# Kernel tuning notes

Hardware: AMD Instinct MI355X
Metric: run time of the kernel (lower is better)

Reference implementation:

```python
import jax, jax.numpy as jnp
import numpy as np

K = 4  # knn_graph(k=4, loop=False) hard-coded in H2GCN.forward


def _knn_2hop_adj(Fet, k):
    """Per-batch kNN graph -> symmetrize -> 2-hop binary adjacency [B,N,N].

    Matches create_adj + get_2hop_neighbors: edge direction and the row
    normalization in create_adj are irrelevant because get_2hop_neighbors
    symmetrizes (adj[row,col]=adj[col,row]=1) and thresholds (adj@adj > 0).
    """
    B, N, _ = Fet.shape
    sq = jnp.sum(Fet * Fet, axis=-1)  # [B,N]
    dist = sq[:, :, None] + sq[:, None, :] - 2.0 * jnp.einsum('bnf,bmf->bnm', Fet, Fet)
    eye = jnp.eye(N, dtype=bool)
    dist = jnp.where(eye[None], jnp.inf, dist)  # loop=False: exclude self
    _, idx = jax.lax.top_k(-dist, k)  # [B,N,k] nearest-neighbor indices
    b_idx = jnp.arange(B)[:, None, None]
    n_idx = jnp.arange(N)[None, :, None]
    A = jnp.zeros((B, N, N), Fet.dtype).at[b_idx, n_idx, idx].set(1.0)
    A = jnp.maximum(A, jnp.swapaxes(A, 1, 2))  # symmetrize 1-hop
    A2 = jnp.einsum('bnm,bmk->bnk', A, A)      # 2-hop counts
    A2 = jnp.where(eye[None], 0.0, A2)          # fill_diagonal_(0)
    return (A2 > 0).astype(Fet.dtype)


def _h2gcn_conv(x, A2, w1, b1, w2, b2):
    """H2GCNConv on dense binary adjacency.

    Dense matmul with binary A2 == gather(x[col]) -> fc2 -> index_add over rows;
    A2.sum(-1) == bincount(row). Degree clamped to >= 1.
    """
    ego = jnp.einsum('bnf,of->bno', x, w1) + b1   # fc1(x)
    msg = jnp.einsum('bnf,of->bno', x, w2) + b2   # fc2(x)
    agg = jnp.einsum('bnm,bmo->bno', A2, msg)     # scatter-add of neighbor msgs
    deg = jnp.maximum(jnp.sum(A2, axis=-1, keepdims=True), 1.0)
    return jax.nn.relu(jnp.concatenate([ego, agg / deg], axis=-1))


def setup_inputs() -> dict:
    key = jax.random.key(0)
    ks = jax.random.split(key, 8)
    B, N, F, NH, NC = 128, 197, 768, 512, 1000
    s = 0.02
    return {
        'Fet': jax.random.normal(ks[0], (B, N, F), jnp.float32),
        'w1_0': jax.random.normal(ks[1], (NH, F), jnp.float32) * s,
        'b1_0': jnp.zeros((NH,), jnp.float32),
        'w2_0': jax.random.normal(ks[2], (NH, F), jnp.float32) * s,
        'b2_0': jnp.zeros((NH,), jnp.float32),
        'w1_1': jax.random.normal(ks[3], (NH, 2 * NH), jnp.float32) * s,
        'b1_1': jnp.zeros((NH,), jnp.float32),
        'w2_1': jax.random.normal(ks[4], (NH, 2 * NH), jnp.float32) * s,
        'b2_1': jnp.zeros((NH,), jnp.float32),
        'fc1_w': jax.random.normal(ks[5], (NH, 4 * NH), jnp.float32) * s,
        'fc1_b': jnp.zeros((NH,), jnp.float32),
        'fc2_w': jax.random.normal(ks[6], (NC, NH), jnp.float32) * s,
        'fc2_b': jnp.zeros((NC,), jnp.float32),
    }


def reference(Fet, w1_0, b1_0, w2_0, b2_0, w1_1, b1_1, w2_1, b2_1,
              fc1_w, fc1_b, fc2_w, fc2_b):
    A2 = _knn_2hop_adj(Fet, K)
    h1 = _h2gcn_conv(Fet, A2, w1_0, b1_0, w2_0, b2_0)   # [B,N,2*nhid]
    h2 = _h2gcn_conv(h1, A2, w1_1, b1_1, w2_1, b2_1)    # [B,N,2*nhid]
    h = jnp.concatenate([h1, h2], axis=-1)              # [B,N,final_dim]
    graph_features = jnp.mean(h, axis=1)                # global_mean_pool
    p = jax.nn.relu(graph_features @ fc1_w.T + fc1_b)   # dropout is identity (eval)
    out = p @ fc2_w.T + fc2_b
    return (out, graph_features)
```

## Files before the change

### kernel.cpp

```cpp
#include <hip/hip_runtime.h>
#include <hip/hip_bf16.h>
#include <math.h>

typedef __attribute__((ext_vector_type(8))) short bf16x8;
typedef __attribute__((ext_vector_type(4))) float f32x4;

#define B_ 128
#define N_ 197
#define F_ 768
#define NH_ 512
#define D2_ 1024
#define D4_ 2048
#define NC_ 1000
#define ROWS_ (B_ * N_)
#define KA_ 224
#define NA_ 256
#define LDG_ 200
#define MT_LD_ (B_ * KA_)

#define OFF_G0     0ull
#define OFF_SQ     20172800ull
#define OFF_ABITS  20273664ull
#define OFF_DEG    21080576ull
#define OFF_FETHI  21181440ull
#define OFF_MSGT   60011520ull
#define OFF_H1     89371648ull
#define OFF_FETLO  OFF_MSGT
#define OFF_POOL   141014016ull
#define OFF_P      142062592ull
#define OFF_WC1    142324736ull
#define OFF_WC2    143897600ull
#define OFF_G1     145994752ull

__device__ __forceinline__ void gll16(const void* g, void* l) {
  __builtin_amdgcn_global_load_lds((const __attribute__((address_space(1))) void*)g,
                                   (__attribute__((address_space(3))) void*)l, 16, 0, 0);
}


__global__ __launch_bounds__(256) void cast_weights(const float* __restrict__ w10,
                                                    const float* __restrict__ w20,
                                                    const float* __restrict__ w11,
                                                    const float* __restrict__ w21,
                                                    __hip_bfloat16* __restrict__ wc1,
                                                    __hip_bfloat16* __restrict__ wc2) {
  const int S1 = NH_ * F_ / 4;
  const int S2 = NH_ * D2_ / 4;
  int i = blockIdx.x * 256 + threadIdx.x;
  const float* src;
  __hip_bfloat16* dst;
  int off;
  if (i < S1) { src = w10; dst = wc1; off = i; }
  else if (i < 2 * S1) { src = w20; dst = wc1 + (size_t)NH_ * F_; off = i - S1; }
  else if (i < 2 * S1 + S2) { src = w11; dst = wc2; off = i - 2 * S1; }
  else { src = w21; dst = wc2 + (size_t)NH_ * D2_; off = i - 2 * S1 - S2; }
  float4 v = ((const float4*)src)[off];
  union { __hip_bfloat16 h[4]; uint2 u; } pk;
  pk.h[0] = __float2bfloat16(v.x);
  pk.h[1] = __float2bfloat16(v.y);
  pk.h[2] = __float2bfloat16(v.z);
  pk.h[3] = __float2bfloat16(v.w);
  ((uint2*)dst)[off] = pk.u;
}

__global__ __launch_bounds__(256) void cast_hilo_sq(const float* __restrict__ X,
                                                    __hip_bfloat16* __restrict__ hi,
                                                    __hip_bfloat16* __restrict__ lo,
                                                    float* __restrict__ sq) {
  int row = blockIdx.x * 4 + (threadIdx.x >> 6);
  int lane = threadIdx.x & 63;
  const float4* xp = (const float4*)(X + (size_t)row * F_);
  uint2* hp = (uint2*)(hi + (size_t)row * F_);
  uint2* lp = (uint2*)(lo + (size_t)row * F_);
  float s = 0.f;
#pragma unroll
  for (int i = 0; i < 3; i++) {
    float4 v = xp[lane + i * 64];
    s += v.x * v.x + v.y * v.y + v.z * v.z + v.w * v.w;
    float f[4] = {v.x, v.y, v.z, v.w};
    union { __hip_bfloat16 h[4]; uint2 u; } ph, pl;
#pragma unroll
    for (int k = 0; k < 4; k++) {
      __hip_bfloat16 h = __float2bfloat16(f[k]);
      ph.h[k] = h;
      pl.h[k] = __float2bfloat16(f[k] - __bfloat162float(h));
    }
    hp[lane + i * 64] = ph.u;
    lp[lane + i * 64] = pl.u;
  }
#pragma unroll
  for (int o = 32; o > 0; o >>= 1) s += __shfl_down(s, o);
  if (lane == 0) sq[row] = s;
}

__global__ __launch_bounds__(256) void mfma_gram(const __hip_bfloat16* __restrict__ Xhi,
                                                 const __hip_bfloat16* __restrict__ Xlo,
                                                 float* __restrict__ g0,
                                                 float* __restrict__ g1) {
  __shared__ short AsH[4096];
  __shared__ short BsH[4096];
  __shared__ short AsL[4096];
  __shared__ short BsL[4096];
  const int t = threadIdx.x;
  const int wgid = blockIdx.x;
  const int L = (wgid & 7) * 96 + (wgid >> 3);
  const int b = L / 6;
  const int rbx = L - b * 6;
  const int bx = rbx % 3;
  const int khalf = rbx / 3;
  const int m0 = (bx == 0) ? 0 : 128;
  const int o0 = (bx == 2) ? 128 : 0;
  const bool mirror = (bx == 1);
  const int l = t & 63, w = t >> 6;
  const int wm = (w >> 1) * 64, wn = (w & 1) * 64;
  const int frow = l & 15, fch = l >> 4;
  const size_t rowbase = (size_t)b * N_;
  const char* AhiB = (const char*)(Xhi + (rowbase + m0) * F_);
  const char* AloB = (const char*)(Xlo + (rowbase + m0) * F_);
  const char* BhiB = (const char*)(Xhi + (rowbase + o0) * F_);
  const char* BloB = (const char*)(Xlo + (rowbase + o0) * F_);
  const int rb = F_ * 2;
  char* AsHB = (char*)AsH;
  char* BsHB = (char*)BsH;
  char* AsLB = (char*)AsL;
  char* BsLB = (char*)BsL;
  float* go = khalf ? g1 : g0;
  f32x4 zero = {0.f, 0.f, 0.f, 0.f};
  f32x4 acc[4][4];
#pragma unroll
  for (int i = 0; i < 4; i++)
#pragma unroll
    for (int j = 0; j < 4; j++) acc[i][j] = zero;
  const int kt0 = khalf * 12;
  for (int kt = kt0; kt < kt0 + 12; kt++) {
    const int kb = kt * 64;
#pragma unroll
    for (int u = 0; u < 2; u++) {
      int prow = u * 32 + (t >> 3);
      int e = (t & 7) ^ (prow & 7);
      int grow = (e >> 2) * 64 + prow;
      size_t goff = (size_t)grow * rb + kb + (e & 3) * 16;
      gll16(AhiB + goff, AsHB + u * 4096 + t * 16);
      gll16(BhiB + goff, BsHB + u * 4096 + t * 16);
      gll16(AloB + goff, AsLB + u * 4096 + t * 16);
      gll16(BloB + goff, BsLB + u * 4096 + t * 16);
    }
    __syncthreads();
    bf16x8 ah[4], al[4], bh[4], bl[4];
#pragma unroll
    for (int i = 0; i < 4; i++) {
      int ar = wm + i * 16 + frow;
      int apr = ar & 63;
      int aoff = apr * 128 + (((((ar >> 6) << 2) | fch) ^ (apr & 7)) * 16);
      ah[i] = *(const bf16x8*)(AsHB + aoff);
      al[i] = *(const bf16x8*)(AsLB + aoff);
      int br = wn + i * 16 + frow;
      int bpr = br & 63;
      int boff = bpr * 128 + (((((br >> 6) << 2) | fch) ^ (bpr & 7)) * 16);
      bh[i] = *(const bf16x8*)(BsHB + boff);
      bl[i] = *(const bf16x8*)(BsLB + boff);
    }
#pragma unroll
    for (int i = 0; i < 4; i++)
#pragma unroll
      for (int j = 0; j < 4; j++) {
        acc[i][j] = __builtin_amdgcn_mfma_f32_16x16x32_bf16(bh[j], ah[i], acc[i][j], 0, 0, 0);
        acc[i][j] = __builtin_amdgcn_mfma_f32_16x16x32_bf16(bl[j], ah[i], acc[i][j], 0, 0, 0);
        acc[i][j] = __builtin_amdgcn_mfma_f32_16x16x32_bf16(bh[j], al[i], acc[i][j], 0, 0, 0);
      }
    __syncthreads();
  }
#pragma unroll
  for (int i = 0; i < 4; i++) {
    int n = m0 + wm + i * 16 + frow;
    if (n >= N_) continue;
    float* gr = go + (rowbase + n) * LDG_;
#pragma unroll
    for (int j = 0; j < 4; j++) {
      int mb = o0 + wn + j * 16 + fch * 4;
      if (mb >= LDG_) continue;
      f32x4 pv = acc[i][j];
      *(f32x4*)&gr[mb] = pv;
      if (mirror) {
#pragma unroll
        for (int r = 0; r < 4; r++)
          go[(rowbase + mb + r) * LDG_ + n] = pv[r];
      }
    }
  }
}

__global__ __launch_bounds__(256) void topk_kernel(const float* __restrict__ g0,
                                                   const float* __restrict__ g1,
                                                   const float* __restrict__ sq,
                                                   unsigned long long* __restrict__ Abits) {
  int row = blockIdx.x * 4 + (threadIdx.x >> 6);
  int lane = threadIdx.x & 63;
  int b = row / N_, n = row - b * N_;
  const float* g0r = g0 + (size_t)row * LDG_;
  const float* g1r = g1 + (size_t)row * LDG_;
  const float* sqb = sq + (size_t)b * N_;
  float v[4];
  int vi[4];
#pragma unroll
  for (int i = 0; i < 4; i++) {
    int m = lane + i * 64;
    bool ok = (m < N_) && (m != n);
    v[i] = ok ? (sqb[m] - 2.f * (g0r[m] + g1r[m])) : INFINITY;
    vi[i] = ok ? m : 0x3fffffff;
  }
  unsigned long long nbr[4] = {0ull, 0ull, 0ull, 0ull};
#pragma unroll
  for (int t = 0; t < 4; t++) {
    float bv = v[0];
    int bi = vi[0];
#pragma unroll
    for (int i = 1; i < 4; i++)
      if (v[i] < bv || (v[i] == bv && vi[i] < bi)) { bv = v[i]; bi = vi[i]; }
#pragma unroll
    for (int o = 1; o < 64; o <<= 1) {
      float ov = __shfl_xor(bv, o);
      int oi = __shfl_xor(bi, o);
      if (ov < bv || (ov == bv && oi < bi)) { bv = ov; bi = oi; }
    }
#pragma unroll
    for (int i = 0; i < 4; i++)
      if (vi[i] == bi) { v[i] = INFINITY; vi[i] = 0x3fffffff; }
    if (lane == 0) {
      nbr[bi >> 6] |= 1ull << (bi & 63);
      atomicOr(&Abits[((size_t)b * N_ + bi) * 4 + (n >> 6)], 1ull << (n & 63));
    }
  }
  if (lane == 0) {
#pragma unroll
    for (int w = 0; w < 4; w++)
      if (nbr[w]) atomicOr(&Abits[(size_t)row * 4 + w], nbr[w]);
  }
}

__global__ __launch_bounds__(256) void a2_kernel(const unsigned long long* __restrict__ Abits,
                                                 __hip_bfloat16* __restrict__ A2bf,
                                                 float* __restrict__ deg) {
  int row = blockIdx.x * 4 + (threadIdx.x >> 6);
  int lane = threadIdx.x & 63;
  int b = row / N_, n = row - b * N_;
  const unsigned long long* arow = Abits + (size_t)row * 4;
  const unsigned long long* base = Abits + (size_t)b * N_ * 4;
  unsigned long long r0 = 0, r1 = 0, r2 = 0, r3 = 0;
#pragma unroll
  for (int w = 0; w < 4; w++) {
    if ((arow[w] >> lane) & 1ull) {
      const unsigned long long* mr = base + (size_t)(w * 64 + lane) * 4;
      r0 |= mr[0]; r1 |= mr[1]; r2 |= mr[2]; r3 |= mr[3];
    }
  }
#pragma unroll
  for (int o = 1; o < 64; o <<= 1) {
    r0 |= __shfl_xor(r0, o);
    r1 |= __shfl_xor(r1, o);
    r2 |= __shfl_xor(r2, o);
    r3 |= __shfl_xor(r3, o);
  }
  unsigned long long rr[4] = {r0, r1, r2, r3};
  rr[n >> 6] &= ~(1ull << (n & 63));
  const int pad = b & 3;
  __hip_bfloat16* out = A2bf + ((size_t)b * NA_ + n) * KA_;
  const __hip_bfloat16 one = __float2bfloat16(1.f);
  const __hip_bfloat16 zer = __float2bfloat16(0.f);
#pragma unroll
  for (int i = 0; i < 4; i++) {
    int m = lane + i * 64;
    if (m < KA_) {
      int k = m - pad;
      bool bit = (k >= 0 && k < N_ && ((rr[k >> 6] >> (k & 63)) & 1ull));
      out[m] = bit ? one : zer;
    }
  }
  if (lane == 0) {
    int dg = __popcll(rr[0]) + __popcll(rr[1]) + __popcll(rr[2]) + __popcll(rr[3]);
    deg[row] = (float)(dg > 0 ? dg : 1);
  }
}

template <int MODE>
__global__ __launch_bounds__(256) void mfma_fused(const __hip_bfloat16* __restrict__ X,
                                                  const __hip_bfloat16* __restrict__ Wcat,
                                                  const float* __restrict__ biasE,
                                                  const float* __restrict__ biasM,
                                                  __hip_bfloat16* __restrict__ h1,
                                                  __hip_bfloat16* __restrict__ msgT,
                                                  float* __restrict__ pool,
                                                  int K) {
  __shared__ short As[2][4096];
  __shared__ short Bs[2][4096];
  const int t = threadIdx.x;
  const int wgid = blockIdx.x;
  const int L = (wgid & 7) * 197 + (wgid >> 3);
  const int m0 = (L >> 3) * 128, o0 = (L & 7) * 128;
  const int l = t & 63, w = t >> 6;
  const int wm = (w >> 1) * 64, wn = (w & 1) * 64;
  const int frow = l & 15, fch = l >> 4;
  const char* Abase = (const char*)(X + (size_t)m0 * K);
  const char* Bbase = (const char*)(Wcat + (size_t)o0 * K);
  const int rb = K * 2;
  char* AsB = (char*)As;
  char* BsB = (char*)Bs;
  const bool ego = (o0 < 512);
  const bool swap = (MODE == 1) && ego;
  const int sp = t >> 3;
  const int se = (t & 7) ^ (sp & 7);
  const size_t goff0 = (size_t)((se >> 2) * 64 + sp) * rb + (se & 3) * 16;
  const size_t goff1 = (size_t)((se >> 2) * 64 + 32 + sp) * rb + (se & 3) * 16;
  auto stage = [&](int buf, int kt) {
    const int kb = kt * 64;
    const int d = buf * 8192 + t * 16;
    gll16(Abase + goff0 + kb, AsB + d);
    gll16(Abase + goff1 + kb, AsB + d + 4096);
    gll16(Bbase + goff0 + kb, BsB + d);
    gll16(Bbase + goff1 + kb, BsB + d + 4096);
  };
  f32x4 zero = {0.f, 0.f, 0.f, 0.f};
  f32x4 acc[4][4];
#pragma unroll
  for (int i = 0; i < 4; i++)
#pragma unroll
    for (int j = 0; j < 4; j++) acc[i][j] = zero;
  const int KT = K >> 5;
  stage(0, 0);
  __syncthreads();
  for (int kt = 0; kt < KT; kt++) {
    const int cur = kt & 1;
    if (kt + 1 < KT) stage(cur ^ 1, kt + 1);
    bf16x8 af[4], bfv[4];
#pragma unroll
    for (int i = 0; i < 4; i++) {
      int ar = wm + i * 16 + frow;
      int apr = ar & 63;
      af[i] = *(const bf16x8*)(AsB + cur * 8192 + apr * 128 +
                               (((((ar >> 6) << 2) | fch) ^ (apr & 7)) * 16));
      int br = wn + i * 16 + frow;
      int bpr = br & 63;
      bfv[i] = *(const bf16x8*)(BsB + cur * 8192 + bpr * 128 +
                                (((((br >> 6) << 2) | fch) ^ (bpr & 7)) * 16));
    }
    if (!swap) {
#pragma unroll
      for (int i = 0; i < 4; i++)
#pragma unroll
        for (int j = 0; j < 4; j++)
          acc[i][j] = __builtin_amdgcn_mfma_f32_16x16x32_bf16(af[i], bfv[j], acc[i][j], 0, 0, 0);
    } else {
#pragma unroll
      for (int i = 0; i < 4; i++)
#pragma unroll
        for (int j = 0; j < 4; j++)
          acc[i][j] = __builtin_amdgcn_mfma_f32_16x16x32_bf16(bfv[j], af[i], acc[i][j], 0, 0, 0);
    }
    __syncthreads();
  }
  if (ego) {
    if (MODE == 1) {
      const int rw = m0 + wm;
      const int b0 = rw / N_;
      const int rloc = (b0 + 1) * N_ - rw;
#pragma unroll
      for (int j = 0; j < 4; j++) {
        int c0 = o0 + wn + j * 16 + fch * 4;
        float4 b4 = *(const float4*)&biasE[c0];
        float bb4[4] = {b4.x, b4.y, b4.z, b4.w};
        float sA4[4] = {0.f, 0.f, 0.f, 0.f};
        float sB4[4] = {0.f, 0.f, 0.f, 0.f};
#pragma unroll
        for (int i = 0; i < 4; i++) {
          int xloc = i * 16 + frow;
          union { __hip_bfloat16 h[4]; uint2 u; } pk;
#pragma unroll
          for (int r = 0; r < 4; r++) {
            float v = fmaxf(acc[i][j][r] + bb4[r], 0.f);
            pk.h[r] = __float2bfloat16(v);
            if (xloc < rloc) sA4[r] += v; else sB4[r] += v;
          }
          *(uint2*)&h1[(size_t)(rw + xloc) * D2_ + c0] = pk.u;
        }
#pragma unroll
        for (int r = 0; r < 4; r++) {
          float sA = sA4[r], sB = sB4[r];
          sA += __shfl_down(sA, 8, 16); sA += __shfl_down(sA, 4, 16);
          sA += __shfl_down(sA, 2, 16); sA += __shfl_down(sA, 1, 16);
          sB += __shfl_down(sB, 8, 16); sB += __shfl_down(sB, 4, 16);
          sB += __shfl_down(sB, 2, 16); sB += __shfl_down(sB, 1, 16);
          if ((l & 15) == 0) {
            atomicAdd(&pool[(size_t)b0 * D4_ + c0 + r], sA);
            if (rloc < 64) atomicAdd(&pool[(size_t)(b0 + 1) * D4_ + c0 + r], sB);
          }
        }
      }
    } else {
#pragma unroll
      for (int j = 0; j < 4; j++) {
        int c = o0 + wn + j * 16 + frow;
        float bv = biasE[c];
        int rw = m0 + wm;
        int b0 = rw / N_;
        int rB = (b0 + 1) * N_;
        float sA = 0.f, sB = 0.f;
#pragma unroll
        for (int i = 0; i < 4; i++) {
          int r0 = m0 + wm + i * 16 + fch * 4;
#pragma unroll
          for (int r = 0; r < 4; r++) {
            float v = fmaxf(acc[i][j][r] + bv, 0.f);
            if (r0 + r < rB) sA += v; else sB += v;
          }
        }
        sA += __shfl_down(sA, 32);
        sA += __shfl_down(sA, 16);
        sB += __shfl_down(sB, 32);
        sB += __shfl_down(sB, 16);
        if (l < 16) {
          atomicAdd(&pool[(size_t)b0 * D4_ + D2_ + c], sA);
          if (rw + 64 > rB) atomicAdd(&pool[(size_t)(b0 + 1) * D4_ + D2_ + c], sB);
        }
      }
    }
  } else {
#pragma unroll
    for (int j = 0; j < 4; j++) {
      int cm = (o0 - 512) + wn + j * 16 + frow;
      float bm = biasM[cm];
      __hip_bfloat16* mrow = msgT + (size_t)cm * MT_LD_;
#pragma unroll
      for (int i = 0; i < 4; i++) {
        int x0 = m0 + wm + i * 16 + fch * 4;
        int b0 = x0 / N_;
        int r0 = x0 - b0 * N_;
        union { __hip_bfloat16 h[4]; uint2 u; } pk;
#pragma unroll
        for (int r = 0; r < 4; r++) pk.h[r] = __float2bfloat16(acc[i][j][r] + bm);
        if (r0 + 3 < N_) {
          *(uint2*)&mrow[b0 * KA_ + (b0 & 3) + r0] = pk.u;
        } else {
#pragma unroll
          for (int r = 0; r < 4; r++) {
            int x = x0 + r;
            int bb = x / N_;
            int rx = x - bb * N_;
            mrow[bb * KA_ + (bb & 3) + rx] = pk.h[r];
          }
        }
      }
    }
  }
}

template <int MODE>
__global__ __launch_bounds__(256) void mfma_agg(const __hip_bfloat16* __restrict__ A2bf,
                                                const __hip_bfloat16* __restrict__ msgT,
                                                const float* __restrict__ deg,
                                                __hip_bfloat16* __restrict__ h1,
                                                float* __restrict__ pool, int poolOff) {
  __shared__ short As[2][4096];
  __shared__ short Bs[2][4096];
  const int t = threadIdx.x;
  const int wgid = blockIdx.x;
  const int L = (wgid & 7) * 128 + (wgid >> 3);
  const int b = L >> 3;
  const int o0 = ((L >> 1) & 3) * 128;
  const int m0 = (L & 1) * 128;
  const int l = t & 63, w = t >> 6;
  const int wm = (w >> 1) * 64, wn = (w & 1) * 64;
  const int frow = l & 15, fch = l >> 4;
  const char* Abase = (const char*)(A2bf + ((size_t)b * NA_ + m0) * KA_);
  const char* Bbase = (const char*)(msgT + (size_t)o0 * MT_LD_ + (size_t)b * KA_);
  char* AsB = (char*)As;
  char* BsB = (char*)Bs;
  const int sp = t >> 3;
  const int se = (t & 7) ^ (sp & 7);
  const int sg0 = (se >> 2) * 64 + sp;
  const int sg1 = sg0 + 32;
  const int sx = (se & 3) * 16;
  auto stage = [&](int buf, int kt) {
    const int kb = kt * 64;
    const int d = buf * 8192 + t * 16;
    gll16(Abase + (size_t)sg0 * (KA_ * 2) + kb + sx, AsB + d);
    gll16(Abase + (size_t)sg1 * (KA_ * 2) + kb + sx, AsB + d + 4096);
    gll16(Bbase + (size_t)sg0 * (MT_LD_ * 2) + kb + sx, BsB + d);
    gll16(Bbase + (size_t)sg1 * (MT_LD_ * 2) + kb + sx, BsB + d + 4096);
  };
  f32x4 zero = {0.f, 0.f, 0.f, 0.f};
  f32x4 acc[4][4];
#pragma unroll
  for (int i = 0; i < 4; i++)
#pragma unroll
    for (int j = 0; j < 4; j++) acc[i][j] = zero;
  stage(0, 0);
  __syncthreads();
  for (int kt = 0; kt < 7; kt++) {
    const int cur = kt & 1;
    if (kt + 1 < 7) stage(cur ^ 1, kt + 1);
    bf16x8 af[4], bfv[4];
#pragma unroll
    for (int i = 0; i < 4; i++) {
      int ar = wm + i * 16 + frow;
      int apr = ar & 63;
      af[i] = *(const bf16x8*)(AsB + cur * 8192 + apr * 128 +
                               (((((ar >> 6) << 2) | fch) ^ (apr & 7)) * 16));
      int br = wn + i * 16 + frow;
      int bpr = br & 63;
      bfv[i] = *(const bf16x8*)(BsB + cur * 8192 + bpr * 128 +
                                (((((br >> 6) << 2) | fch) ^ (bpr & 7)) * 16));
    }
#pragma unroll
    for (int i = 0; i < 4; i++)
#pragma unroll
      for (int j = 0; j < 4; j++)
        acc[i][j] = __builtin_amdgcn_mfma_f32_16x16x32_bf16(bfv[j], af[i], acc[i][j], 0, 0, 0);
    __syncthreads();
  }
  float sv[4][4];
#pragma unroll
  for (int j = 0; j < 4; j++)
#pragma unroll
    for (int r = 0; r < 4; r++) sv[j][r] = 0.f;
#pragma unroll
  for (int i = 0; i < 4; i++) {
    int n = m0 + wm + i * 16 + frow;
    bool ok = (n < N_);
    float dinv = ok ? (1.f / deg[b * N_ + n]) : 0.f;
#pragma unroll
    for (int j = 0; j < 4; j++) {
      int c0 = o0 + wn + j * 16 + fch * 4;
      union { __hip_bfloat16 h[4]; uint2 u; } pk;
#pragma unroll
      for (int r = 0; r < 4; r++) {
        float v = ok ? fmaxf(acc[i][j][r] * dinv, 0.f) : 0.f;
        sv[j][r] += v;
        pk.h[r] = __float2bfloat16(v);
      }
      if (MODE == 0 && ok)
        *(uint2*)&h1[((size_t)b * N_ + n) * D2_ + NH_ + c0] = pk.u;
    }
  }
#pragma unroll
  for (int j = 0; j < 4; j++) {
#pragma unroll
    for (int r = 0; r < 4; r++) {
      float s = sv[j][r];
      s += __shfl_down(s, 8, 16);
      s += __shfl_down(s, 4, 16);
      s += __shfl_down(s, 2, 16);
      s += __shfl_down(s, 1, 16);
      if ((l & 15) == 0)
        atomicAdd(&pool[(size_t)b * D4_ + poolOff + o0 + wn + j * 16 + fch * 4 + r], s);
    }
  }
}

__global__ __launch_bounds__(256) void scale_pool(const float* __restrict__ pool,
                                                  float* __restrict__ gf) {
  int b = blockIdx.y;
  int c = blockIdx.x * 256 + threadIdx.x;
  gf[(size_t)b * D4_ + c] = pool[(size_t)b * D4_ + c] * (1.f / N_);
}

template <bool RELUX>
__global__ __launch_bounds__(256) void head_gemm(const float* __restrict__ Xg,
                                                 const float* __restrict__ W,
                                                 const float* __restrict__ bias,
                                                 float* __restrict__ Y,
                                                 int Rows, int Fin, int O, int kchunk) {
  __shared__ float Xs[16][68];
  __shared__ float Ws[16][68];
  int tx = threadIdx.x, ty = threadIdx.y;
  int tid = ty * 16 + tx;
  int lr = tid >> 2;
  int lk = (tid & 3) * 4;
  int rbase = blockIdx.y * 64;
  int o0 = blockIdx.x * 64;
  int k0base = blockIdx.z * kchunk;
  float acc[4][4] = {};
  for (int k0 = k0base; k0 < k0base + kchunk; k0 += 16) {
    float4 xv = make_float4(0.f, 0.f, 0.f, 0.f);
    if (rbase + lr < Rows) xv = *(const float4*)&Xg[(size_t)(rbase + lr) * Fin + k0 + lk];
    if (RELUX) {
      xv.x = fmaxf(xv.x, 0.f); xv.y = fmaxf(xv.y, 0.f);
      xv.z = fmaxf(xv.z, 0.f); xv.w = fmaxf(xv.w, 0.f);
    }
    Xs[lk][lr] = xv.x; Xs[lk + 1][lr] = xv.y; Xs[lk + 2][lr] = xv.z; Xs[lk + 3][lr] = xv.w;
    float4 wv = make_float4(0.f, 0.f, 0.f, 0.f);
    if (o0 + lr < O) wv = *(const float4*)&W[(size_t)(o0 + lr) * Fin + k0 + lk];
    Ws[lk][lr] = wv.x; Ws[lk + 1][lr] = wv.y; Ws[lk + 2][lr] = wv.z; Ws[lk + 3][lr] = wv.w;
    __syncthreads();
#pragma unroll
    for (int k = 0; k < 16; k++) {
      float4 a = *(const float4*)&Xs[k][ty * 4];
      float4 bb = *(const float4*)&Ws[k][tx * 4];
      float av[4] = {a.x, a.y, a.z, a.w};
      float bv[4] = {bb.x, bb.y, bb.z, bb.w};
#pragma unroll
      for (int i = 0; i < 4; i++)
#pragma unroll
        for (int j = 0; j < 4; j++) acc[i][j] = fmaf(av[i], bv[j], acc[i][j]);
    }
    __syncthreads();
  }
#pragma unroll
  for (int i = 0; i < 4; i++) {
    int rrow = rbase + ty * 4 + i;
    if (rrow >= Rows) continue;
#pragma unroll
    for (int j = 0; j < 4; j++) {
      int c = o0 + tx * 4 + j;
      if (c >= O) continue;
      float vv = acc[i][j] + ((blockIdx.z == 0) ? bias[c] : 0.f);
      atomicAdd(&Y[(size_t)rrow * O + c], vv);
    }
  }
}

extern "C" void kernel_launch(void* const* d_in, const int* in_sizes, int n_in,
                              void* d_out, int out_size, void* d_ws, size_t ws_size,
                              hipStream_t stream) {
  const float* Fet  = (const float*)d_in[0];
  const float* w1_0 = (const float*)d_in[1];
  const float* b1_0 = (const float*)d_in[2];
  const float* w2_0 = (const float*)d_in[3];
  const float* b2_0 = (const float*)d_in[4];
  const float* w1_1 = (const float*)d_in[5];
  const float* b1_1 = (const float*)d_in[6];
  const float* w2_1 = (const float*)d_in[7];
  const float* b2_1 = (const float*)d_in[8];
  const float* fc1_w = (const float*)d_in[9];
  const float* fc1_b = (const float*)d_in[10];
  const float* fc2_w = (const float*)d_in[11];
  const float* fc2_b = (const float*)d_in[12];

  char* ws = (char*)d_ws;
  float* g0 = (float*)(ws + OFF_G0);
  float* g1 = (float*)(ws + OFF_G1);
  __hip_bfloat16* A2bf = (__hip_bfloat16*)(ws + OFF_G0);
  float* sq = (float*)(ws + OFF_SQ);
  unsigned long long* Abits = (unsigned long long*)(ws + OFF_ABITS);
  float* deg = (float*)(ws + OFF_DEG);
  __hip_bfloat16* Fet_hi = (__hip_bfloat16*)(ws + OFF_FETHI);
  __hip_bfloat16* Fet_lo = (__hip_bfloat16*)(ws + OFF_FETLO);
  __hip_bfloat16* msgT = (__hip_bfloat16*)(ws + OFF_MSGT);
  __hip_bfloat16* h1 = (__hip_bfloat16*)(ws + OFF_H1);
  float* pool = (float*)(ws + OFF_POOL);
  float* p = (float*)(ws + OFF_P);
  __hip_bfloat16* wc1 = (__hip_bfloat16*)(ws + OFF_WC1);
  __hip_bfloat16* wc2 = (__hip_bfloat16*)(ws + OFF_WC2);

  float* out = (float*)d_out;
  float* gf = out + (size_t)B_ * NC_;

  hipMemsetAsync(Abits, 0, (size_t)ROWS_ * 4 * sizeof(unsigned long long), stream);
  hipMemsetAsync(pool, 0, (size_t)B_ * D4_ * sizeof(float), stream);
  hipMemsetAsync(p, 0, (size_t)B_ * NH_ * sizeof(float), stream);
  hipMemsetAsync(out, 0, (size_t)B_ * NC_ * sizeof(float), stream);

  cast_hilo_sq<<<ROWS_ / 4, 256, 0, stream>>>(Fet, Fet_hi, Fet_lo, sq);
  cast_weights<<<1792, 256, 0, stream>>>(w1_0, w2_0, w1_1, w2_1, wc1, wc2);

  mfma_gram<<<768, 256, 0, stream>>>(Fet_hi, Fet_lo, g0, g1);
  topk_kernel<<<ROWS_ / 4, 256, 0, stream>>>(g0, g1, sq, Abits);
  a2_kernel<<<ROWS_ / 4, 256, 0, stream>>>(Abits, A2bf, deg);

  mfma_fused<1><<<1576, 256, 0, stream>>>(Fet_hi, wc1, b1_0, b2_0, h1, msgT, pool, F_);
  mfma_agg<0><<<1024, 256, 0, stream>>>(A2bf, msgT, deg, h1, pool, NH_);

  mfma_fused<2><<<1576, 256, 0, stream>>>(h1, wc2, b1_1, b2_1, nullptr, msgT, pool, D2_);
  mfma_agg<1><<<1024, 256, 0, stream>>>(A2bf, msgT, deg, nullptr, pool, D2_ + NH_);

  scale_pool<<<dim3(8, B_), 256, 0, stream>>>(pool, gf);

  head_gemm<false><<<dim3(8, 2, 16), dim3(16, 16), 0, stream>>>(
      gf, fc1_w, fc1_b, p, B_, D4_, NH_, 128);
  head_gemm<true><<<dim3(16, 2, 8), dim3(16, 16), 0, stream>>>(
      p, fc2_w, fc2_b, out, B_, NH_, NC_, 64);
}
```

Baseline: 440.7 us.

## Enlarge fused GEMM tiles to 256x256 with 8 waves and interleaved prefetch

```diff
diff --git a/kernel.cpp b/kernel.cpp
--- a/kernel.cpp
+++ b/kernel.cpp
@@ -13,6 +13,8 @@
 #define D4_ 2048
 #define NC_ 1000
 #define ROWS_ (B_ * N_)
+#define MPAD_ 25344
+#define GRIDM_ 99
 #define KA_ 224
 #define NA_ 256
 #define LDG_ 200
@@ -23,20 +25,19 @@
 #define OFF_ABITS  20273664ull
 #define OFF_DEG    21080576ull
 #define OFF_FETHI  21181440ull
-#define OFF_MSGT   60011520ull
-#define OFF_H1     89371648ull
+#define OFF_MSGT   60109824ull
+#define OFF_H1     89469952ull
 #define OFF_FETLO  OFF_MSGT
-#define OFF_POOL   141014016ull
-#define OFF_P      142062592ull
-#define OFF_WC1    142324736ull
-#define OFF_WC2    143897600ull
-#define OFF_G1     145994752ull
+#define OFF_POOL   141374464ull
+#define OFF_P      142423040ull
+#define OFF_WC1    142685184ull
+#define OFF_WC2    144258048ull
+#define OFF_G1     146355200ull
 
 __device__ __forceinline__ void gll16(const void* g, void* l) {
   __builtin_amdgcn_global_load_lds((const __attribute__((address_space(1))) void*)g,
                                    (__attribute__((address_space(3))) void*)l, 16, 0, 0);
 }
-
 
 __global__ __launch_bounds__(256) void cast_weights(const float* __restrict__ w10,
                                                     const float* __restrict__ w20,
@@ -283,23 +284,27 @@
 }
 
 template <int MODE>
-__global__ __launch_bounds__(256) void mfma_fused(const __hip_bfloat16* __restrict__ X,
-                                                  const __hip_bfloat16* __restrict__ Wcat,
-                                                  const float* __restrict__ biasE,
-                                                  const float* __restrict__ biasM,
-                                                  __hip_bfloat16* __restrict__ h1,
-                                                  __hip_bfloat16* __restrict__ msgT,
-                                                  float* __restrict__ pool,
-                                                  int K) {
-  __shared__ short As[2][4096];
-  __shared__ short Bs[2][4096];
+__global__ __launch_bounds__(512) void mfma_fused8(const __hip_bfloat16* __restrict__ X,
+                                                   const __hip_bfloat16* __restrict__ Wcat,
+                                                   const float* __restrict__ biasE,
+                                                   const float* __restrict__ biasM,
+                                                   __hip_bfloat16* __restrict__ h1,
+                                                   __hip_bfloat16* __restrict__ msgT,
+                                                   float* __restrict__ pool,
+                                                   int K) {
+  __shared__ short As[2][16384];
+  __shared__ short Bs[2][16384];
   const int t = threadIdx.x;
-  const int wgid = blockIdx.x;
-  const int L = (wgid & 7) * 197 + (wgid >> 3);
-  const int m0 = (L >> 3) * 128, o0 = (L & 7) * 128;
+  const int nwg = GRIDM_ * 4;
+  const int q = nwg >> 3, r8 = nwg & 7;
+  const int xcd = blockIdx.x & 7, rk = blockIdx.x >> 3;
+  const int L = (xcd < r8 ? xcd * (q + 1) : r8 * (q + 1) + (xcd - r8) * q) + rk;
+  const int m0 = (L >> 2) * 256, o0 = (L & 3) * 256;
   const int l = t & 63, w = t >> 6;
-  const int wm = (w >> 1) * 64, wn = (w & 1) * 64;
+  const int wm = (w >> 2) * 128;
+  const int wn = (w & 3) * 64;
   const int frow = l & 15, fch = l >> 4;
+  const int cb = o0 + wn;
   const char* Abase = (const char*)(X + (size_t)m0 * K);
   const char* Bbase = (const char*)(Wcat + (size_t)o0 * K);
   const int rb = K * 2;
@@ -309,40 +314,52 @@
   const bool swap = (MODE == 1) && ego;
   const int sp = t >> 3;
   const int se = (t & 7) ^ (sp & 7);
-  const size_t goff0 = (size_t)((se >> 2) * 64 + sp) * rb + (se & 3) * 16;
-  const size_t goff1 = (size_t)((se >> 2) * 64 + 32 + sp) * rb + (se & 3) * 16;
-  auto stage = [&](int buf, int kt) {
-    const int kb = kt * 64;
-    const int d = buf * 8192 + t * 16;
-    gll16(Abase + goff0 + kb, AsB + d);
-    gll16(Abase + goff1 + kb, AsB + d + 4096);
-    gll16(Bbase + goff0 + kb, BsB + d);
-    gll16(Bbase + goff1 + kb, BsB + d + 4096);
-  };
+  const int sx = se * 16;
   f32x4 zero = {0.f, 0.f, 0.f, 0.f};
-  f32x4 acc[4][4];
-#pragma unroll
-  for (int i = 0; i < 4; i++)
+  f32x4 acc[8][4];
+#pragma unroll
+  for (int i = 0; i < 8; i++)
 #pragma unroll
     for (int j = 0; j < 4; j++) acc[i][j] = zero;
-  const int KT = K >> 5;
-  stage(0, 0);
-  __syncthreads();
+  const int KT = K >> 6;
+#pragma unroll
+  for (int u = 0; u < 4; u++)
+    gll16(Abase + (size_t)(u * 64 + sp) * rb + sx, AsB + u * 8192 + t * 16);
+#pragma unroll
+  for (int u = 0; u < 4; u++)
+    gll16(Bbase + (size_t)(u * 64 + sp) * rb + sx, BsB + u * 8192 + t * 16);
+
   for (int kt = 0; kt < KT; kt++) {
     const int cur = kt & 1;
-    if (kt + 1 < KT) stage(cur ^ 1, kt + 1);
-    bf16x8 af[4], bfv[4];
+    const int nb = cur ^ 1;
+    const size_t kbn = (size_t)(kt + 1) * 128;
+    const bool hasNext = (kt + 1 < KT);
+    char* Ac = AsB + cur * 32768;
+    char* Bc = BsB + cur * 32768;
+    char* An = AsB + nb * 32768;
+    char* Bn = BsB + nb * 32768;
+    if (hasNext) {
+      gll16(Abase + (size_t)(0 * 64 + sp) * rb + kbn + sx, An + 0 * 8192 + t * 16);
+      gll16(Abase + (size_t)(1 * 64 + sp) * rb + kbn + sx, An + 1 * 8192 + t * 16);
+      asm volatile("s_waitcnt vmcnt(2)" ::: "memory");
+    } else {
+      asm volatile("s_waitcnt vmcnt(0)" ::: "memory");
+    }
+    __builtin_amdgcn_sched_barrier(0);
+    __builtin_amdgcn_s_barrier();
+    __builtin_amdgcn_sched_barrier(0);
+    bf16x8 bfv[4], af[4];
+#pragma unroll
+    for (int j = 0; j < 4; j++) {
+      int br = wn + j * 16 + frow;
+      bfv[j] = *(const bf16x8*)(Bc + br * 128 + ((fch ^ (br & 7)) * 16));
+    }
 #pragma unroll
     for (int i = 0; i < 4; i++) {
       int ar = wm + i * 16 + frow;
-      int apr = ar & 63;
-      af[i] = *(const bf16x8*)(AsB + cur * 8192 + apr * 128 +
-                               (((((ar >> 6) << 2) | fch) ^ (apr & 7)) * 16));
-      int br = wn + i * 16 + frow;
-      int bpr = br & 63;
-      bfv[i] = *(const bf16x8*)(BsB + cur * 8192 + bpr * 128 +
-                                (((((br >> 6) << 2) | fch) ^ (bpr & 7)) * 16));
-    }
+      af[i] = *(const bf16x8*)(Ac + ar * 128 + ((fch ^ (ar & 7)) * 16));
+    }
+    __builtin_amdgcn_s_setprio(1);
     if (!swap) {
 #pragma unroll
       for (int i = 0; i < 4; i++)
@@ -356,22 +373,103 @@
         for (int j = 0; j < 4; j++)
           acc[i][j] = __builtin_amdgcn_mfma_f32_16x16x32_bf16(bfv[j], af[i], acc[i][j], 0, 0, 0);
     }
-    __syncthreads();
-  }
+    __builtin_amdgcn_s_setprio(0);
+    if (hasNext) {
+      gll16(Abase + (size_t)(2 * 64 + sp) * rb + kbn + sx, An + 2 * 8192 + t * 16);
+      gll16(Abase + (size_t)(3 * 64 + sp) * rb + kbn + sx, An + 3 * 8192 + t * 16);
+    }
+#pragma unroll
+    for (int i = 0; i < 4; i++) {
+      int ar = wm + (i + 4) * 16 + frow;
+      af[i] = *(const bf16x8*)(Ac + ar * 128 + ((fch ^ (ar & 7)) * 16));
+    }
+    __builtin_amdgcn_s_setprio(1);
+    if (!swap) {
+#pragma unroll
+      for (int i = 0; i < 4; i++)
+#pragma unroll
+        for (int j = 0; j < 4; j++)
+          acc[i + 4][j] = __builtin_amdgcn_mfma_f32_16x16x32_bf16(af[i], bfv[j], acc[i + 4][j], 0, 0, 0);
+    } else {
+#pragma unroll
+      for (int i = 0; i < 4; i++)
+#pragma unroll
+        for (int j = 0; j < 4; j++)
+          acc[i + 4][j] = __builtin_amdgcn_mfma_f32_16x16x32_bf16(bfv[j], af[i], acc[i + 4][j], 0, 0, 0);
+    }
+    __builtin_amdgcn_s_setprio(0);
+    if (hasNext) {
+      gll16(Bbase + (size_t)(0 * 64 + sp) * rb + kbn + sx, Bn + 0 * 8192 + t * 16);
+      gll16(Bbase + (size_t)(1 * 64 + sp) * rb + kbn + sx, Bn + 1 * 8192 + t * 16);
+    }
+#pragma unroll
+    for (int j = 0; j < 4; j++) {
+      int br = wn + j * 16 + frow;
+      bfv[j] = *(const bf16x8*)(Bc + br * 128 + (((4 + fch) ^ (br & 7)) * 16));
+    }
+#pragma unroll
+    for (int i = 0; i < 4; i++) {
+      int ar = wm + i * 16 + frow;
+      af[i] = *(const bf16x8*)(Ac + ar * 128 + (((4 + fch) ^ (ar & 7)) * 16));
+    }
+    __builtin_amdgcn_s_setprio(1);
+    if (!swap) {
+#pragma unroll
+      for (int i = 0; i < 4; i++)
+#pragma unroll
+        for (int j = 0; j < 4; j++)
+          acc[i][j] = __builtin_amdgcn_mfma_f32_16x16x32_bf16(af[i], bfv[j], acc[i][j], 0, 0, 0);
+    } else {
+#pragma unroll
+      for (int i = 0; i < 4; i++)
+#pragma unroll
+        for (int j = 0; j < 4; j++)
+          acc[i][j] = __builtin_amdgcn_mfma_f32_16x16x32_bf16(bfv[j], af[i], acc[i][j], 0, 0, 0);
+    }
+    __builtin_amdgcn_s_setprio(0);
+    if (hasNext) {
+      gll16(Bbase + (size_t)(2 * 64 + sp) * rb + kbn + sx, Bn + 2 * 8192 + t * 16);
+      gll16(Bbase + (size_t)(3 * 64 + sp) * rb + kbn + sx, Bn + 3 * 8192 + t * 16);
+    }
+#pragma unroll
+    for (int i = 0; i < 4; i++) {
+      int ar = wm + (i + 4) * 16 + frow;
+      af[i] = *(const bf16x8*)(Ac + ar * 128 + (((4 + fch) ^ (ar & 7)) * 16));
+    }
+    __builtin_amdgcn_s_setprio(1);
+    if (!swap) {
+#pragma unroll
+      for (int i = 0; i < 4; i++)
+#pragma unroll
+        for (int j = 0; j < 4; j++)
+          acc[i + 4][j] = __builtin_amdgcn_mfma_f32_16x16x32_bf16(af[i], bfv[j], acc[i + 4][j], 0, 0, 0);
+    } else {
+#pragma unroll
+      for (int i = 0; i < 4; i++)
+#pragma unroll
+        for (int j = 0; j < 4; j++)
+          acc[i + 4][j] = __builtin_amdgcn_mfma_f32_16x16x32_bf16(bfv[j], af[i], acc[i + 4][j], 0, 0, 0);
+    }
+    __builtin_amdgcn_s_setprio(0);
+    __builtin_amdgcn_s_barrier();
+    __builtin_amdgcn_sched_barrier(0);
+  }
+
+  const int rw = m0 + wm;
+  if (rw >= ROWS_) return;
   if (ego) {
     if (MODE == 1) {
-      const int rw = m0 + wm;
       const int b0 = rw / N_;
       const int rloc = (b0 + 1) * N_ - rw;
 #pragma unroll
       for (int j = 0; j < 4; j++) {
-        int c0 = o0 + wn + j * 16 + fch * 4;
+        int c0 = cb + j * 16 + fch * 4;
         float4 b4 = *(const float4*)&biasE[c0];
         float bb4[4] = {b4.x, b4.y, b4.z, b4.w};
         float sA4[4] = {0.f, 0.f, 0.f, 0.f};
         float sB4[4] = {0.f, 0.f, 0.f, 0.f};
 #pragma unroll
-        for (int i = 0; i < 4; i++) {
+        for (int i = 0; i < 8; i++) {
           int xloc = i * 16 + frow;
           union { __hip_bfloat16 h[4]; uint2 u; } pk;
 #pragma unroll
@@ -391,22 +489,21 @@
           sB += __shfl_down(sB, 2, 16); sB += __shfl_down(sB, 1, 16);
           if ((l & 15) == 0) {
             atomicAdd(&pool[(size_t)b0 * D4_ + c0 + r], sA);
-            if (rloc < 64) atomicAdd(&pool[(size_t)(b0 + 1) * D4_ + c0 + r], sB);
+            if (rloc < 128) atomicAdd(&pool[(size_t)(b0 + 1) * D4_ + c0 + r], sB);
           }
         }
       }
     } else {
+      const int b0 = rw / N_;
+      const int rB = (b0 + 1) * N_;
 #pragma unroll
       for (int j = 0; j < 4; j++) {
-        int c = o0 + wn + j * 16 + frow;
+        int c = cb + j * 16 + frow;
         float bv = biasE[c];
-        int rw = m0 + wm;
-        int b0 = rw / N_;
-        int rB = (b0 + 1) * N_;
         float sA = 0.f, sB = 0.f;
 #pragma unroll
-        for (int i = 0; i < 4; i++) {
-          int r0 = m0 + wm + i * 16 + fch * 4;
+        for (int i = 0; i < 8; i++) {
+          int r0 = rw + i * 16 + fch * 4;
 #pragma unroll
           for (int r = 0; r < 4; r++) {
             float v = fmaxf(acc[i][j][r] + bv, 0.f);
@@ -419,19 +516,19 @@
         sB += __shfl_down(sB, 16);
         if (l < 16) {
           atomicAdd(&pool[(size_t)b0 * D4_ + D2_ + c], sA);
-          if (rw + 64 > rB) atomicAdd(&pool[(size_t)(b0 + 1) * D4_ + D2_ + c], sB);
+          if (rw + 128 > rB) atomicAdd(&pool[(size_t)(b0 + 1) * D4_ + D2_ + c], sB);
         }
       }
     }
   } else {
 #pragma unroll
     for (int j = 0; j < 4; j++) {
-      int cm = (o0 - 512) + wn + j * 16 + frow;
+      int cm = (cb - 512) + j * 16 + frow;
       float bm = biasM[cm];
       __hip_bfloat16* mrow = msgT + (size_t)cm * MT_LD_;
 #pragma unroll
-      for (int i = 0; i < 4; i++) {
-        int x0 = m0 + wm + i * 16 + fch * 4;
+      for (int i = 0; i < 8; i++) {
+        int x0 = rw + i * 16 + fch * 4;
         int b0 = x0 / N_;
         int r0 = x0 - b0 * N_;
         union { __hip_bfloat16 h[4]; uint2 u; } pk;
@@ -666,10 +763,10 @@
   topk_kernel<<<ROWS_ / 4, 256, 0, stream>>>(g0, g1, sq, Abits);
   a2_kernel<<<ROWS_ / 4, 256, 0, stream>>>(Abits, A2bf, deg);
 
-  mfma_fused<1><<<1576, 256, 0, stream>>>(Fet_hi, wc1, b1_0, b2_0, h1, msgT, pool, F_);
+  mfma_fused8<1><<<GRIDM_ * 4, 512, 0, stream>>>(Fet_hi, wc1, b1_0, b2_0, h1, msgT, pool, F_);
   mfma_agg<0><<<1024, 256, 0, stream>>>(A2bf, msgT, deg, h1, pool, NH_);
 
-  mfma_fused<2><<<1576, 256, 0, stream>>>(h1, wc2, b1_1, b2_1, nullptr, msgT, pool, D2_);
+  mfma_fused8<2><<<GRIDM_ * 4, 512, 0, stream>>>(h1, wc2, b1_1, b2_1, nullptr, msgT, pool, D2_);
   mfma_agg<1><<<1024, 256, 0, stream>>>(A2bf, msgT, deg, nullptr, pool, D2_ + NH_);
 
   scale_pool<<<dim3(8, B_), 256, 0, stream>>>(pool, gf);
```

Result: slower. 560.4 us (+27.2%).
